# Kernel tuning notes

Hardware: AMD Instinct MI355X
Metric: run time of the kernel (lower is better)

## Reference

```python
import jax, jax.numpy as jnp
import numpy as np

B = 2048
D = 256
C = 100000
SCALE = 30.0
MARGIN = 0.2
EPS = 1e-6


def setup_inputs() -> dict:
    key = jax.random.key(0)
    k1, k2, k3 = jax.random.split(key, 3)
    emb = jax.random.normal(k1, (B, D), dtype=jnp.float32)
    # speaker embeddings are typically L2-normalized; also keeps cosines in (-1,1)
    emb = emb / jnp.linalg.norm(emb, axis=1, keepdims=True)
    W = jax.random.normal(k2, (C, D), dtype=jnp.float32)
    targets = jax.random.randint(k3, (B,), 0, C, dtype=jnp.int64)
    return {"embedding": emb, "W": W, "targets": targets}


def reference(embedding, W, targets):
    # normalize classifier rows (F.normalize on weight, dim=1, eps=1e-12)
    Wn = W / jnp.maximum(jnp.linalg.norm(W, axis=1, keepdims=True), 1e-12)
    # [B, C] cosine logits, clamped as in the original
    cos = jnp.clip(embedding @ Wn.T, -1.0, 1.0)
    # per-sample target cosine -> margin-adjusted numerator
    tgt_cos = jnp.take_along_axis(cos, targets[:, None], axis=1)[:, 0]
    numerator = SCALE * jnp.cos(jnp.arccos(tgt_cos) + MARGIN)  # [B]
    # masked sum over non-target classes (replaces the python loop + cat)
    col = jnp.arange(C, dtype=targets.dtype)[None, :]
    not_target = (col != targets[:, None]).astype(cos.dtype)  # [B, C]
    excl_sum = jnp.sum(jnp.exp(SCALE * cos) * not_target, axis=1)  # [B]
    denominator = jnp.exp(numerator) + excl_sum
    loss = -jnp.mean(numerator - jnp.log(denominator + EPS))
    return loss
```

## Files before the change

### kernel.cpp

```cpp
#include <hip/hip_runtime.h>
#include <hip/hip_bf16.h>


static constexpr int Bn = 2048;
static constexpr int Dn = 256;
static constexpr int Cn = 100000;
static constexpr int NCBLK  = 782;
static constexpr int CPAD   = NCBLK * 128;
static constexpr int SLICES = NCBLK * 4;
static constexpr float OOB_COLS = (float)(CPAD - Cn);
static constexpr int NTILE = Bn / 32;

#define SCALE_F 30.0f
#define MARGIN_F 0.2f
#define EPS_F 1e-6f

typedef __attribute__((ext_vector_type(8))) short bf16x8;
typedef __attribute__((ext_vector_type(4))) float f32x4;
typedef __attribute__((address_space(3))) unsigned int lds_u32;
typedef const __attribute__((address_space(1))) unsigned int g_u32;

__device__ __forceinline__ void async_cp16(const void* g, void* lds) {
    __builtin_amdgcn_global_load_lds((g_u32*)g, (lds_u32*)lds, 16, 0, 0);
}

__device__ __forceinline__ short f2bf_rne(float x) {
    union { float f; unsigned int u; } v; v.f = x;
    unsigned int r = v.u + 0x7fffu + ((v.u >> 16) & 1u);
    return (short)(r >> 16);
}

__global__ __launch_bounds__(256) void k_prep(const float* __restrict__ W,
                                              const float* __restrict__ emb,
                                              const int* __restrict__ tgt,
                                              short* __restrict__ embbf,
                                              float* __restrict__ numv,
                                              float* __restrict__ etv) {
    const int blk = blockIdx.x;
    if (blk < 512) {
        const int i = (blk * 256 + threadIdx.x) * 4;
        float4 x = *(const float4*)(emb + i);
        short4 o;
        o.x = f2bf_rne(x.x); o.y = f2bf_rne(x.y);
        o.z = f2bf_rne(x.z); o.w = f2bf_rne(x.w);
        *(short4*)(embbf + i) = o;
    } else {
        const int b    = (blk - 512) * 4 + (threadIdx.x >> 6);
        const int lane = threadIdx.x & 63;
        const int t    = tgt[b];
        float4 x = *(const float4*)(W + (size_t)t * Dn + lane * 4);
        float4 e = *(const float4*)(emb + b * Dn + lane * 4);
        float dot = x.x * e.x + x.y * e.y + x.z * e.z + x.w * e.w;
        float ss  = x.x * x.x + x.y * x.y + x.z * x.z + x.w * x.w;
#pragma unroll
        for (int o = 1; o < 64; o <<= 1) {
            dot += __shfl_xor(dot, o);
            ss  += __shfl_xor(ss, o);
        }
        if (lane == 0) {
            float cosv = dot / fmaxf(sqrtf(ss), 1e-12f);
            cosv = fminf(fmaxf(cosv, -1.f), 1.f);
            const float num = SCALE_F * cosf(acosf(cosv) + MARGIN_F);
            numv[b] = num;
            etv[b]  = __expf(SCALE_F * cosv);
        }
    }
}

__global__ __launch_bounds__(256, 4) void k_main(const float* __restrict__ W,
                                                 const short* __restrict__ embbf,
                                                 float* __restrict__ partial) {
    __shared__ __align__(16) short stage[2 * 32 * 256];

    const int tid  = threadIdx.x;
    const int wave = tid >> 6;
    const int lane = tid & 63;
    const int q    = lane >> 4;
    const int cr   = lane & 15;
    const int sw   = cr & 7;

    const int cblk  = blockIdx.x;
    const int cbase = cblk * 128 + wave * 32;

    auto stage_tile = [&](int t, int buf) {
        short* dst = stage + buf * (32 * 256);
#pragma unroll
        for (int i = 0; i < 4; ++i) {
            const int r0 = wave * 8 + 2 * i;
            const int rl = r0 + (lane >> 5);
            const int c16 = (lane & 31) ^ (rl & 7);
            const short* g = embbf + (size_t)(t * 32 + rl) * Dn + c16 * 8;
            async_cp16(g, dst + r0 * 256);
        }
    };

    stage_tile(0, 0);

    bf16x8 afrag[2][8];
#pragma unroll
    for (int ct = 0; ct < 2; ++ct) {
        const int c = cbase + ct * 16 + cr;
        const float* wr = W + (size_t)c * Dn;
        float ss = 0.0f;
        if (c < Cn) {
#pragma unroll
            for (int ks = 0; ks < 8; ++ks) {
                float4 x0 = *(const float4*)(wr + ks * 32 + q * 8);
                float4 x1 = *(const float4*)(wr + ks * 32 + q * 8 + 4);
                ss += x0.x * x0.x + x0.y * x0.y + x0.z * x0.z + x0.w * x0.w;
                ss += x1.x * x1.x + x1.y * x1.y + x1.z * x1.z + x1.w * x1.w;
            }
        }
        ss += __shfl_xor(ss, 16);
        ss += __shfl_xor(ss, 32);
        const float rn = 1.0f / fmaxf(sqrtf(ss), 1e-12f);
#pragma unroll
        for (int ks = 0; ks < 8; ++ks) {
            bf16x8 a = {0, 0, 0, 0, 0, 0, 0, 0};
            if (c < Cn) {
                float4 x0 = *(const float4*)(wr + ks * 32 + q * 8);
                float4 x1 = *(const float4*)(wr + ks * 32 + q * 8 + 4);
                a[0] = f2bf_rne(x0.x * rn); a[1] = f2bf_rne(x0.y * rn);
                a[2] = f2bf_rne(x0.z * rn); a[3] = f2bf_rne(x0.w * rn);
                a[4] = f2bf_rne(x1.x * rn); a[5] = f2bf_rne(x1.y * rn);
                a[6] = f2bf_rne(x1.z * rn); a[7] = f2bf_rne(x1.w * rn);
            }
            afrag[ct][ks] = a;
        }
    }

    __syncthreads();

    float* pout = partial + (size_t)(cblk * 4 + wave) * Bn;

    for (int it = 0; it < NTILE; ++it) {
        const int buf = it & 1;
        if (it + 1 < NTILE) stage_tile(it + 1, buf ^ 1);

        const short* sb = stage + buf * (32 * 256);
#pragma unroll
        for (int st = 0; st < 2; ++st) {
            const short* rowp = sb + (st * 16 + cr) * 256;
            f32x4 acc0 = {0.f, 0.f, 0.f, 0.f};
            f32x4 acc1 = {0.f, 0.f, 0.f, 0.f};
#pragma unroll
            for (int half = 0; half < 2; ++half) {
                bf16x8 bf[4];
#pragma unroll
                for (int j = 0; j < 4; ++j) {
                    const int ks = half * 4 + j;
                    bf[j] = *(const bf16x8*)(rowp + ((((ks << 2) | q) ^ sw) << 3));
                }
#pragma unroll
                for (int j = 0; j < 4; ++j) {
                    const int ks = half * 4 + j;
                    acc0 = __builtin_amdgcn_mfma_f32_16x16x32_bf16(afrag[0][ks], bf[j], acc0, 0, 0, 0);
                    acc1 = __builtin_amdgcn_mfma_f32_16x16x32_bf16(afrag[1][ks], bf[j], acc1, 0, 0, 0);
                }
            }

            float s = 0.0f;
#pragma unroll
            for (int r = 0; r < 4; ++r) {
                s += __expf(SCALE_F * acc0[r]);
                s += __expf(SCALE_F * acc1[r]);
            }
            s += __shfl_xor(s, 16);
            s += __shfl_xor(s, 32);
            if (lane < 16) pout[it * 32 + st * 16 + cr] = s;
        }
        __syncthreads();
    }
}

static constexpr int SCHUNK = 98;
__global__ __launch_bounds__(256) void k_rowsum(const float* __restrict__ partial,
                                                float* __restrict__ rowsum) {
    const int b  = blockIdx.x * 256 + threadIdx.x;
    const int s0 = blockIdx.y * SCHUNK;
    const int s1 = min(s0 + SCHUNK, SLICES);
    float acc = 0.0f;
    for (int s = s0; s < s1; ++s) acc += partial[(size_t)s * Bn + b];
    atomicAdd(&rowsum[b], acc);
}

__global__ __launch_bounds__(256) void k_loss(const float* __restrict__ numv,
                                              const float* __restrict__ etv,
                                              const float* __restrict__ rowsum,
                                              float* __restrict__ out) {
    float acc = 0.0f;
    for (int b = threadIdx.x; b < Bn; b += 256) {
        const float num  = numv[b];
        const float excl = rowsum[b] - OOB_COLS - etv[b];
        const float denom = __expf(num) + excl;
        acc += num - logf(denom + EPS_F);
    }
#pragma unroll
    for (int o = 1; o < 64; o <<= 1) acc += __shfl_xor(acc, o);
    __shared__ float sa[4];
    const int wave = threadIdx.x >> 6, lane = threadIdx.x & 63;
    if (lane == 0) sa[wave] = acc;
    __syncthreads();
    if (threadIdx.x == 0) out[0] = -(sa[0] + sa[1] + sa[2] + sa[3]) / (float)Bn;
}

extern "C" void kernel_launch(void* const* d_in, const int* in_sizes, int n_in,
                              void* d_out, int out_size, void* d_ws, size_t ws_size,
                              hipStream_t stream) {
    const float* emb = (const float*)d_in[0];
    const float* W   = (const float*)d_in[1];
    const int*   tgt = (const int*)d_in[2];
    float* out = (float*)d_out;

    char* ws = (char*)d_ws;
    short* embbf   = (short*)ws;
    float* partial = (float*)(ws + (1 << 20));
    float* rowsum  = partial + (size_t)SLICES * Bn;
    float* numv    = rowsum + Bn;
    float* etv     = numv + Bn;

    hipMemsetAsync(rowsum, 0, Bn * sizeof(float), stream);
    k_prep<<<1024, 256, 0, stream>>>(W, emb, tgt, embbf, numv, etv);
    k_main<<<NCBLK, 256, 0, stream>>>(W, embbf, partial);
    k_rowsum<<<dim3(Bn / 256, 32), 256, 0, stream>>>(partial, rowsum);
    k_loss<<<1, 256, 0, stream>>>(numv, etv, rowsum, out);
}
```

Baseline: 309.2 us.

## Pre-swizzle embeddings into MFMA fragment layout and stream them from global memory

The prep kernel now writes the bf16 embedding directly in per-lane MFMA B-fragment order, so the main kernel loads fragments straight from global/L2 into registers with double buffering and no LDS staging or barriers. The main kernel becomes one wave per block handling 64 classes (four A fragments), doubling MFMA work per B load. The rowsum and loss kernels are merged into a single finish kernel that reduces in LDS and accumulates into the output atomically, replacing the rowsum memset. Risks include higher register pressure from 32 A fragments plus 16 B fragments, reliance on L2 for embedding reuse, and far fewer finish blocks reducing each partial column serially.

```diff
diff --git a/kernel.cpp b/kernel.cpp
--- a/kernel.cpp
+++ b/kernel.cpp
@@ -5,11 +5,10 @@
 static constexpr int Bn = 2048;
 static constexpr int Dn = 256;
 static constexpr int Cn = 100000;
-static constexpr int NCBLK  = 782;
-static constexpr int CPAD   = NCBLK * 128;
-static constexpr int SLICES = NCBLK * 4;
+static constexpr int NSLICE = 1564;
+static constexpr int CPAD   = NSLICE * 64;
 static constexpr float OOB_COLS = (float)(CPAD - Cn);
-static constexpr int NTILE = Bn / 32;
+static constexpr int NT = Bn / 16;
 
 #define SCALE_F 30.0f
 #define MARGIN_F 0.2f
@@ -17,12 +16,6 @@
 
 typedef __attribute__((ext_vector_type(8))) short bf16x8;
 typedef __attribute__((ext_vector_type(4))) float f32x4;
-typedef __attribute__((address_space(3))) unsigned int lds_u32;
-typedef const __attribute__((address_space(1))) unsigned int g_u32;
-
-__device__ __forceinline__ void async_cp16(const void* g, void* lds) {
-    __builtin_amdgcn_global_load_lds((g_u32*)g, (lds_u32*)lds, 16, 0, 0);
-}
 
 __device__ __forceinline__ short f2bf_rne(float x) {
     union { float f; unsigned int u; } v; v.f = x;
@@ -33,19 +26,28 @@
 __global__ __launch_bounds__(256) void k_prep(const float* __restrict__ W,
                                               const float* __restrict__ emb,
                                               const int* __restrict__ tgt,
-                                              short* __restrict__ embbf,
+                                              short* __restrict__ embF,
                                               float* __restrict__ numv,
                                               float* __restrict__ etv) {
     const int blk = blockIdx.x;
-    if (blk < 512) {
-        const int i = (blk * 256 + threadIdx.x) * 4;
-        float4 x = *(const float4*)(emb + i);
-        short4 o;
-        o.x = f2bf_rne(x.x); o.y = f2bf_rne(x.y);
-        o.z = f2bf_rne(x.z); o.w = f2bf_rne(x.w);
-        *(short4*)(embbf + i) = o;
+    if (blk < 256) {
+        const int t     = blk >> 1;
+        const int chunk = (blk & 1) * 256 + threadIdx.x;
+        const int ks    = chunk >> 6;
+        const int lane  = chunk & 63;
+        const int q     = lane >> 4;
+        const int cr    = lane & 15;
+        const float* src = emb + (size_t)(t * 16 + cr) * Dn + ks * 32 + q * 8;
+        float4 x0 = *(const float4*)(src);
+        float4 x1 = *(const float4*)(src + 4);
+        bf16x8 o;
+        o[0] = f2bf_rne(x0.x); o[1] = f2bf_rne(x0.y);
+        o[2] = f2bf_rne(x0.z); o[3] = f2bf_rne(x0.w);
+        o[4] = f2bf_rne(x1.x); o[5] = f2bf_rne(x1.y);
+        o[6] = f2bf_rne(x1.z); o[7] = f2bf_rne(x1.w);
+        *(bf16x8*)(embF + (size_t)((t * 8 + ks) * 64 + lane) * 8) = o;
     } else {
-        const int b    = (blk - 512) * 4 + (threadIdx.x >> 6);
+        const int b    = (blk - 256) * 4 + (threadIdx.x >> 6);
         const int lane = threadIdx.x & 63;
         const int t    = tgt[b];
         float4 x = *(const float4*)(W + (size_t)t * Dn + lane * 4);
@@ -67,38 +69,18 @@
     }
 }
 
-__global__ __launch_bounds__(256, 4) void k_main(const float* __restrict__ W,
-                                                 const short* __restrict__ embbf,
-                                                 float* __restrict__ partial) {
-    __shared__ __align__(16) short stage[2 * 32 * 256];
-
-    const int tid  = threadIdx.x;
-    const int wave = tid >> 6;
-    const int lane = tid & 63;
+__global__ __launch_bounds__(64, 2) void k_main(const float* __restrict__ W,
+                                                const short* __restrict__ embF,
+                                                float* __restrict__ partial) {
+    const int lane = threadIdx.x;
     const int q    = lane >> 4;
     const int cr   = lane & 15;
-    const int sw   = cr & 7;
-
-    const int cblk  = blockIdx.x;
-    const int cbase = cblk * 128 + wave * 32;
-
-    auto stage_tile = [&](int t, int buf) {
-        short* dst = stage + buf * (32 * 256);
-#pragma unroll
-        for (int i = 0; i < 4; ++i) {
-            const int r0 = wave * 8 + 2 * i;
-            const int rl = r0 + (lane >> 5);
-            const int c16 = (lane & 31) ^ (rl & 7);
-            const short* g = embbf + (size_t)(t * 32 + rl) * Dn + c16 * 8;
-            async_cp16(g, dst + r0 * 256);
-        }
-    };
-
-    stage_tile(0, 0);
-
-    bf16x8 afrag[2][8];
-#pragma unroll
-    for (int ct = 0; ct < 2; ++ct) {
+    const int sl   = blockIdx.x;
+    const int cbase = sl * 64;
+
+    bf16x8 afrag[4][8];
+#pragma unroll
+    for (int ct = 0; ct < 4; ++ct) {
         const int c = cbase + ct * 16 + cr;
         const float* wr = W + (size_t)c * Dn;
         float ss = 0.0f;
@@ -129,79 +111,78 @@
         }
     }
 
+    float* pout = partial + (size_t)sl * Bn;
+    const bf16x8* bsrc = (const bf16x8*)embF;
+
+    auto load_b = [&](bf16x8* bf, int t) {
+        const bf16x8* p = bsrc + (size_t)t * 512 + lane;
+#pragma unroll
+        for (int ks = 0; ks < 8; ++ks) bf[ks] = p[ks * 64];
+    };
+
+    auto compute = [&](const bf16x8* bf, int t) {
+        f32x4 a0 = {0.f, 0.f, 0.f, 0.f};
+        f32x4 a1 = {0.f, 0.f, 0.f, 0.f};
+        f32x4 a2 = {0.f, 0.f, 0.f, 0.f};
+        f32x4 a3 = {0.f, 0.f, 0.f, 0.f};
+#pragma unroll
+        for (int ks = 0; ks < 8; ++ks) {
+            a0 = __builtin_amdgcn_mfma_f32_16x16x32_bf16(afrag[0][ks], bf[ks], a0, 0, 0, 0);
+            a1 = __builtin_amdgcn_mfma_f32_16x16x32_bf16(afrag[1][ks], bf[ks], a1, 0, 0, 0);
+            a2 = __builtin_amdgcn_mfma_f32_16x16x32_bf16(afrag[2][ks], bf[ks], a2, 0, 0, 0);
+            a3 = __builtin_amdgcn_mfma_f32_16x16x32_bf16(afrag[3][ks], bf[ks], a3, 0, 0, 0);
+        }
+        float s = 0.0f;
+#pragma unroll
+        for (int r = 0; r < 4; ++r) {
+            s += __expf(SCALE_F * a0[r]);
+            s += __expf(SCALE_F * a1[r]);
+            s += __expf(SCALE_F * a2[r]);
+            s += __expf(SCALE_F * a3[r]);
+        }
+        s += __shfl_xor(s, 16);
+        s += __shfl_xor(s, 32);
+        if (lane < 16) pout[t * 16 + cr] = s;
+    };
+
+    bf16x8 b0[8], b1[8];
+    load_b(b0, 0);
+    for (int t = 0; t < NT; t += 2) {
+        load_b(b1, t + 1);
+        compute(b0, t);
+        load_b(b0, (t + 2) < NT ? (t + 2) : 0);
+        compute(b1, t + 1);
+    }
+}
+
+__global__ __launch_bounds__(256) void k_finish(const float* __restrict__ partial,
+                                                const float* __restrict__ numv,
+                                                const float* __restrict__ etv,
+                                                float* __restrict__ out) {
+    __shared__ float red[64];
+    const int l  = threadIdx.x & 63;
+    const int qq = threadIdx.x >> 6;
+    const int b  = blockIdx.x * 64 + l;
+
+    if (threadIdx.x < 64) red[threadIdx.x] = 0.0f;
     __syncthreads();
 
-    float* pout = partial + (size_t)(cblk * 4 + wave) * Bn;
-
-    for (int it = 0; it < NTILE; ++it) {
-        const int buf = it & 1;
-        if (it + 1 < NTILE) stage_tile(it + 1, buf ^ 1);
-
-        const short* sb = stage + buf * (32 * 256);
-#pragma unroll
-        for (int st = 0; st < 2; ++st) {
-            const short* rowp = sb + (st * 16 + cr) * 256;
-            f32x4 acc0 = {0.f, 0.f, 0.f, 0.f};
-            f32x4 acc1 = {0.f, 0.f, 0.f, 0.f};
-#pragma unroll
-            for (int half = 0; half < 2; ++half) {
-                bf16x8 bf[4];
-#pragma unroll
-                for (int j = 0; j < 4; ++j) {
-                    const int ks = half * 4 + j;
-                    bf[j] = *(const bf16x8*)(rowp + ((((ks << 2) | q) ^ sw) << 3));
-                }
-#pragma unroll
-                for (int j = 0; j < 4; ++j) {
-                    const int ks = half * 4 + j;
-                    acc0 = __builtin_amdgcn_mfma_f32_16x16x32_bf16(afrag[0][ks], bf[j], acc0, 0, 0, 0);
-                    acc1 = __builtin_amdgcn_mfma_f32_16x16x32_bf16(afrag[1][ks], bf[j], acc1, 0, 0, 0);
-                }
-            }
-
-            float s = 0.0f;
-#pragma unroll
-            for (int r = 0; r < 4; ++r) {
-                s += __expf(SCALE_F * acc0[r]);
-                s += __expf(SCALE_F * acc1[r]);
-            }
-            s += __shfl_xor(s, 16);
-            s += __shfl_xor(s, 32);
-            if (lane < 16) pout[it * 32 + st * 16 + cr] = s;
-        }
-        __syncthreads();
-    }
-}
-
-static constexpr int SCHUNK = 98;
-__global__ __launch_bounds__(256) void k_rowsum(const float* __restrict__ partial,
-                                                float* __restrict__ rowsum) {
-    const int b  = blockIdx.x * 256 + threadIdx.x;
-    const int s0 = blockIdx.y * SCHUNK;
-    const int s1 = min(s0 + SCHUNK, SLICES);
+    const int s0 = qq * (NSLICE / 4);
+    const int s1 = s0 + (NSLICE / 4);
     float acc = 0.0f;
     for (int s = s0; s < s1; ++s) acc += partial[(size_t)s * Bn + b];
-    atomicAdd(&rowsum[b], acc);
-}
-
-__global__ __launch_bounds__(256) void k_loss(const float* __restrict__ numv,
-                                              const float* __restrict__ etv,
-                                              const float* __restrict__ rowsum,
-                                              float* __restrict__ out) {
-    float acc = 0.0f;
-    for (int b = threadIdx.x; b < Bn; b += 256) {
+    atomicAdd(&red[l], acc);
+    __syncthreads();
+
+    if (threadIdx.x < 64) {
         const float num  = numv[b];
-        const float excl = rowsum[b] - OOB_COLS - etv[b];
+        const float excl = red[l] - OOB_COLS - etv[b];
         const float denom = __expf(num) + excl;
-        acc += num - logf(denom + EPS_F);
-    }
-#pragma unroll
-    for (int o = 1; o < 64; o <<= 1) acc += __shfl_xor(acc, o);
-    __shared__ float sa[4];
-    const int wave = threadIdx.x >> 6, lane = threadIdx.x & 63;
-    if (lane == 0) sa[wave] = acc;
-    __syncthreads();
-    if (threadIdx.x == 0) out[0] = -(sa[0] + sa[1] + sa[2] + sa[3]) / (float)Bn;
+        float term = num - logf(denom + EPS_F);
+#pragma unroll
+        for (int o = 1; o < 64; o <<= 1) term += __shfl_xor(term, o);
+        if (l == 0) atomicAdd(out, -term / (float)Bn);
+    }
 }
 
 extern "C" void kernel_launch(void* const* d_in, const int* in_sizes, int n_in,
@@ -213,15 +194,13 @@
     float* out = (float*)d_out;
 
     char* ws = (char*)d_ws;
-    short* embbf   = (short*)ws;
+    short* embF    = (short*)ws;
     float* partial = (float*)(ws + (1 << 20));
-    float* rowsum  = partial + (size_t)SLICES * Bn;
-    float* numv    = rowsum + Bn;
+    float* numv    = partial + (size_t)NSLICE * Bn;
     float* etv     = numv + Bn;
 
-    hipMemsetAsync(rowsum, 0, Bn * sizeof(float), stream);
-    k_prep<<<1024, 256, 0, stream>>>(W, emb, tgt, embbf, numv, etv);
-    k_main<<<NCBLK, 256, 0, stream>>>(W, embbf, partial);
-    k_rowsum<<<dim3(Bn / 256, 32), 256, 0, stream>>>(partial, rowsum);
-    k_loss<<<1, 256, 0, stream>>>(numv, etv, rowsum, out);
-}
+    hipMemsetAsync(out, 0, sizeof(float), stream);
+    k_prep<<<768, 256, 0, stream>>>(W, emb, tgt, embF, numv, etv);
+    k_main<<<NSLICE, 64, 0, stream>>>(W, embF, partial);
+    k_finish<<<32, 256, 0, stream>>>(partial, numv, etv, out);
+}
```

After: 274.2 us. 11.3% less time.
